# Kernel optimization log

Hardware: AMD Instinct MI355X
Metric: run time of the kernel (lower is better)

## Reference

```python
import jax, jax.numpy as jnp
import numpy as np

N, X_DIM, Y_DIM, HID = 1024, 128, 128, 256


def setup_inputs() -> dict:
    key = jax.random.key(0)
    ks = jax.random.split(key, 4)
    x = jax.random.normal(ks[0], (N, X_DIM), dtype=jnp.float32)
    y = jax.random.normal(ks[1], (N, Y_DIM), dtype=jnp.float32)
    # PyTorch Linear default init scale ~ 1/sqrt(fan_in)
    W1 = jax.random.normal(ks[2], (X_DIM + Y_DIM, HID), dtype=jnp.float32) / np.sqrt(X_DIM + Y_DIM)
    b1 = jnp.zeros((HID,), dtype=jnp.float32)
    W2 = jax.random.normal(ks[3], (HID, 1), dtype=jnp.float32) / np.sqrt(HID)
    b2 = jnp.zeros((1,), dtype=jnp.float32)
    return {"x_samples": x, "y_samples": y, "W1": W1, "b1": b1, "W2": W2, "b2": b2}


def reference(x_samples, y_samples, W1, b1, W2, b2):
    n = y_samples.shape[0]
    x_dim = x_samples.shape[-1]
    # F(concat(x, y)) on the diagonal pairs -> T0: [N, 1]
    xy = jnp.concatenate([x_samples, y_samples], axis=-1)
    T0 = jax.nn.relu(xy @ W1 + b1) @ W2 + b2
    # Pairwise term without materializing the [N, N, x+y] concat:
    # T1[i, j] = F(concat(x[j], y[i])) - 1. Split W1 into x- and y-blocks and
    # broadcast-sum the two small projections before the ReLU.
    Wx, Wy = W1[:x_dim], W1[x_dim:]
    xp = x_samples @ Wx  # [N, HID]
    yp = y_samples @ Wy  # [N, HID]
    h = jax.nn.relu(xp[None, :, :] + yp[:, None, :] + b1)  # [N, N, HID]
    T1 = h @ W2 + b2 - 1.0  # [N, N, 1]
    lse = jax.nn.logsumexp(T1, axis=1)  # [N, 1]
    lower_bound = T0.mean() - jnp.exp(lse - jnp.log(jnp.float32(n))).mean()
    return lower_bound
```

## Files before the change

### kernel.cpp

```cpp
#include <hip/hip_runtime.h>


#define N_S   1024
#define XD    128
#define HIDD  256
#define JBLK  16
#define IBLK  8
#define JTILE 256

__global__ __launch_bounds__(256) void proj_kernel(
    const float* __restrict__ x, const float* __restrict__ y,
    const float* __restrict__ W1, const float* __restrict__ b1,
    float* __restrict__ At, float* __restrict__ Yp) {
  const int k     = threadIdx.x;
  const int which = blockIdx.y;
  const int r0    = blockIdx.x * JBLK;

  __shared__ float s_in[JBLK][XD];
  const float* src = which ? y : x;
  for (int t = k; t < JBLK * XD; t += 256)
    s_in[t >> 7][t & 127] = src[r0 * XD + t];
  __syncthreads();

  const float* W = W1 + (which ? XD * HIDD : 0);
  float acc[JBLK];
  #pragma unroll
  for (int r = 0; r < JBLK; ++r) acc[r] = 0.f;

  #pragma unroll 4
  for (int d = 0; d < XD; ++d) {
    const float w = W[d * HIDD + k];
    #pragma unroll
    for (int r = 0; r < JBLK; ++r)
      acc[r] = fmaf(s_in[r][d], w, acc[r]);
  }

  if (which) {
    #pragma unroll
    for (int r = 0; r < JBLK; ++r) Yp[(r0 + r) * HIDD + k] = acc[r];
  } else {
    const float bk = b1[k];
    __shared__ float s_t[HIDD][JBLK + 1];
    #pragma unroll
    for (int r = 0; r < JBLK; ++r) s_t[k][r] = acc[r] + bk;
    __syncthreads();
    const int jj = k & (JBLK - 1);
    const int kk = k >> 4;
    #pragma unroll
    for (int m = 0; m < JBLK; ++m) {
      const int kr = m * 16 + kk;
      At[kr * N_S + r0 + jj] = s_t[kr][jj];
    }
  }
}

__global__ __launch_bounds__(256, 2) void pair_kernel(
    const float* __restrict__ At, const float* __restrict__ Yp,
    const float* __restrict__ W2, const float* __restrict__ b2,
    float2* __restrict__ partial) {
  const int tid = threadIdx.x;
  const int ib  = blockIdx.x >> 2;
  const int jt  = blockIdx.x & 3;
  const int i0  = ib * IBLK;
  const int j   = jt * JTILE + tid;

  __shared__ float s_row[HIDD][12];
  #pragma unroll
  for (int ii = 0; ii < IBLK; ++ii)
    s_row[tid][ii] = Yp[(i0 + ii) * HIDD + tid];
  s_row[tid][8] = W2[tid];
  __syncthreads();

  float acc[IBLK];
  #pragma unroll
  for (int ii = 0; ii < IBLK; ++ii) acc[ii] = 0.f;

  const float* ap = At + j;
  #pragma unroll 4
  for (int k = 0; k < HIDD; ++k) {
    const float  a  = ap[k * N_S];
    const float4 y0 = *(const float4*)&s_row[k][0];
    const float4 y1 = *(const float4*)&s_row[k][4];
    const float  w  = s_row[k][8];
    acc[0] = fmaf(fmaxf(a + y0.x, 0.f), w, acc[0]);
    acc[1] = fmaf(fmaxf(a + y0.y, 0.f), w, acc[1]);
    acc[2] = fmaf(fmaxf(a + y0.z, 0.f), w, acc[2]);
    acc[3] = fmaf(fmaxf(a + y0.w, 0.f), w, acc[3]);
    acc[4] = fmaf(fmaxf(a + y1.x, 0.f), w, acc[4]);
    acc[5] = fmaf(fmaxf(a + y1.y, 0.f), w, acc[5]);
    acc[6] = fmaf(fmaxf(a + y1.z, 0.f), w, acc[6]);
    acc[7] = fmaf(fmaxf(a + y1.w, 0.f), w, acc[7]);
  }

  const float bb = b2[0] - 1.0f;
  float esum = 0.f;
  #pragma unroll
  for (int ii = 0; ii < IBLK; ++ii) esum += __expf(acc[ii] + bb);

  float diag = 0.f;
  const int dd = j - i0;
  #pragma unroll
  for (int ii = 0; ii < IBLK; ++ii)
    if (dd == ii) diag = acc[ii];

  #pragma unroll
  for (int m = 32; m >= 1; m >>= 1) {
    esum += __shfl_xor(esum, m, 64);
    diag += __shfl_xor(diag, m, 64);
  }
  __shared__ float s_es[4], s_dg[4];
  const int wave = tid >> 6, lane = tid & 63;
  if (lane == 0) { s_es[wave] = esum; s_dg[wave] = diag; }
  __syncthreads();
  if (tid == 0)
    partial[blockIdx.x] = make_float2(s_es[0] + s_es[1] + s_es[2] + s_es[3],
                                      s_dg[0] + s_dg[1] + s_dg[2] + s_dg[3]);
}

__global__ __launch_bounds__(256) void finalize_kernel(
    const float2* __restrict__ partial, const float* __restrict__ b2,
    float* __restrict__ out) {
  const int tid = threadIdx.x;
  const float2 p0 = partial[tid];
  const float2 p1 = partial[tid + 256];
  double es = (double)p0.x + (double)p1.x;
  double dg = (double)p0.y + (double)p1.y;
  #pragma unroll
  for (int m = 32; m >= 1; m >>= 1) {
    es += __shfl_xor(es, m, 64);
    dg += __shfl_xor(dg, m, 64);
  }
  __shared__ double s_es[4], s_dg[4];
  const int wave = tid >> 6, lane = tid & 63;
  if (lane == 0) { s_es[wave] = es; s_dg[wave] = dg; }
  __syncthreads();
  if (tid == 0) {
    const double esT = s_es[0] + s_es[1] + s_es[2] + s_es[3];
    const double dgT = s_dg[0] + s_dg[1] + s_dg[2] + s_dg[3];
    const double n = (double)N_S;
    out[0] = (float)(dgT / n + (double)b2[0] - esT / (n * n));
  }
}

extern "C" void kernel_launch(void* const* d_in, const int* in_sizes, int n_in,
                              void* d_out, int out_size, void* d_ws, size_t ws_size,
                              hipStream_t stream) {
  const float* x  = (const float*)d_in[0];
  const float* y  = (const float*)d_in[1];
  const float* W1 = (const float*)d_in[2];
  const float* b1 = (const float*)d_in[3];
  const float* W2 = (const float*)d_in[4];
  const float* b2 = (const float*)d_in[5];

  float*  At      = (float*)d_ws;
  float*  Yp      = At + HIDD * N_S;
  float2* partial = (float2*)(Yp + N_S * HIDD);

  dim3 g1(N_S / JBLK, 2);
  proj_kernel<<<g1, 256, 0, stream>>>(x, y, W1, b1, At, Yp);
  pair_kernel<<<(N_S / IBLK) * (N_S / JTILE), 256, 0, stream>>>(At, Yp, W2, b2, partial);
  finalize_kernel<<<1, 256, 0, stream>>>(partial, b2, (float*)d_out);
}
```

Measured before the change: 107.3 us.

## Split ReLU into rank-one and abs terms, read Y projections via scalar loads

Uses relu(z) = 0.5*(z + |z|) so the linear part of the pairwise MLP becomes a rank-one term R[j] + C[i]. A new small kernel precomputes R and C as dot products with W2. The inner loop then does only an add plus an FMA with an abs operand modifier, instead of add, max and FMA. The y-projection is now stored transposed and read straight from global memory with block-uniform addresses, replacing the LDS staging; occupancy is raised to 4 blocks per SIMD. The cost is an extra kernel launch and a small extra pass over the projections.

```diff
diff --git a/kernel.cpp b/kernel.cpp
--- a/kernel.cpp
+++ b/kernel.cpp
@@ -1,17 +1,18 @@
 #include <hip/hip_runtime.h>
 
 
-#define N_S   1024
-#define XD    128
-#define HIDD  256
-#define JBLK  16
-#define IBLK  8
-#define JTILE 256
+#define N_S  1024
+#define XD   128
+#define HIDD 256
+#define JBLK 8
+#define IBLK 8
+#define JT   256
+#define JPT  1
 
 __global__ __launch_bounds__(256) void proj_kernel(
     const float* __restrict__ x, const float* __restrict__ y,
     const float* __restrict__ W1, const float* __restrict__ b1,
-    float* __restrict__ At, float* __restrict__ Yp) {
+    float* __restrict__ At, float* __restrict__ YpT) {
   const int k     = threadIdx.x;
   const int which = blockIdx.y;
   const int r0    = blockIdx.x * JBLK;
@@ -35,73 +36,77 @@
       acc[r] = fmaf(s_in[r][d], w, acc[r]);
   }
 
-  if (which) {
-    #pragma unroll
-    for (int r = 0; r < JBLK; ++r) Yp[(r0 + r) * HIDD + k] = acc[r];
-  } else {
-    const float bk = b1[k];
-    __shared__ float s_t[HIDD][JBLK + 1];
-    #pragma unroll
-    for (int r = 0; r < JBLK; ++r) s_t[k][r] = acc[r] + bk;
-    __syncthreads();
-    const int jj = k & (JBLK - 1);
-    const int kk = k >> 4;
-    #pragma unroll
-    for (int m = 0; m < JBLK; ++m) {
-      const int kr = m * 16 + kk;
-      At[kr * N_S + r0 + jj] = s_t[kr][jj];
-    }
+  const float bk = which ? 0.f : b1[k];
+  float* dst = which ? YpT : At;
+  __shared__ float s_t[HIDD][JBLK + 1];
+  #pragma unroll
+  for (int r = 0; r < JBLK; ++r) s_t[k][r] = acc[r] + bk;
+  __syncthreads();
+  const int jj = k & (JBLK - 1);
+  const int kk = k >> 3;
+  #pragma unroll
+  for (int m = 0; m < JBLK; ++m) {
+    const int kr = m * 32 + kk;
+    dst[kr * N_S + r0 + jj] = s_t[kr][jj];
   }
 }
 
-__global__ __launch_bounds__(256, 2) void pair_kernel(
-    const float* __restrict__ At, const float* __restrict__ Yp,
-    const float* __restrict__ W2, const float* __restrict__ b2,
+__global__ __launch_bounds__(256) void rank1_kernel(
+    const float* __restrict__ At, const float* __restrict__ YpT,
+    const float* __restrict__ W2, float* __restrict__ R, float* __restrict__ C) {
+  const int b = blockIdx.x;
+  const int j = (b & 3) * 256 + threadIdx.x;
+  const float* src = (b < 4) ? At : YpT;
+  float s0 = 0.f, s1 = 0.f, s2 = 0.f, s3 = 0.f;
+  #pragma unroll 4
+  for (int k = 0; k < HIDD; k += 4) {
+    s0 = fmaf(src[(k + 0) * N_S + j], W2[k + 0], s0);
+    s1 = fmaf(src[(k + 1) * N_S + j], W2[k + 1], s1);
+    s2 = fmaf(src[(k + 2) * N_S + j], W2[k + 2], s2);
+    s3 = fmaf(src[(k + 3) * N_S + j], W2[k + 3], s3);
+  }
+  ((b < 4) ? R : C)[j] = (s0 + s1) + (s2 + s3);
+}
+
+__global__ __launch_bounds__(256, 4) void pair2_kernel(
+    const float* __restrict__ At, const float* __restrict__ YpT,
+    const float* __restrict__ W2, const float* __restrict__ R,
+    const float* __restrict__ C, const float* __restrict__ b2,
     float2* __restrict__ partial) {
   const int tid = threadIdx.x;
   const int ib  = blockIdx.x >> 2;
   const int jt  = blockIdx.x & 3;
   const int i0  = ib * IBLK;
-  const int j   = jt * JTILE + tid;
-
-  __shared__ float s_row[HIDD][12];
-  #pragma unroll
-  for (int ii = 0; ii < IBLK; ++ii)
-    s_row[tid][ii] = Yp[(i0 + ii) * HIDD + tid];
-  s_row[tid][8] = W2[tid];
-  __syncthreads();
+  const int j   = jt * JT + tid;
 
   float acc[IBLK];
   #pragma unroll
   for (int ii = 0; ii < IBLK; ++ii) acc[ii] = 0.f;
 
   const float* ap = At + j;
-  #pragma unroll 4
+  #pragma unroll 8
   for (int k = 0; k < HIDD; ++k) {
-    const float  a  = ap[k * N_S];
-    const float4 y0 = *(const float4*)&s_row[k][0];
-    const float4 y1 = *(const float4*)&s_row[k][4];
-    const float  w  = s_row[k][8];
-    acc[0] = fmaf(fmaxf(a + y0.x, 0.f), w, acc[0]);
-    acc[1] = fmaf(fmaxf(a + y0.y, 0.f), w, acc[1]);
-    acc[2] = fmaf(fmaxf(a + y0.z, 0.f), w, acc[2]);
-    acc[3] = fmaf(fmaxf(a + y0.w, 0.f), w, acc[3]);
-    acc[4] = fmaf(fmaxf(a + y1.x, 0.f), w, acc[4]);
-    acc[5] = fmaf(fmaxf(a + y1.y, 0.f), w, acc[5]);
-    acc[6] = fmaf(fmaxf(a + y1.z, 0.f), w, acc[6]);
-    acc[7] = fmaf(fmaxf(a + y1.w, 0.f), w, acc[7]);
+    const float a = ap[k * N_S];
+    const float w = W2[k];
+    const float* cr = YpT + k * N_S + i0;
+    #pragma unroll
+    for (int ii = 0; ii < IBLK; ++ii) {
+      const float z = a + cr[ii];
+      acc[ii] = fmaf(fabsf(z), w, acc[ii]);
+    }
   }
 
   const float bb = b2[0] - 1.0f;
-  float esum = 0.f;
-  #pragma unroll
-  for (int ii = 0; ii < IBLK; ++ii) esum += __expf(acc[ii] + bb);
-
-  float diag = 0.f;
+  const float Rj = R[j];
+  float esum = 0.f, diag = 0.f;
   const int dd = j - i0;
   #pragma unroll
-  for (int ii = 0; ii < IBLK; ++ii)
-    if (dd == ii) diag = acc[ii];
+  for (int ii = 0; ii < IBLK; ++ii) {
+    const float Ci = C[i0 + ii];
+    const float t  = fmaf(0.5f, Rj + Ci + acc[ii], bb);
+    esum += __expf(t);
+    if (ii == dd) diag += t;
+  }
 
   #pragma unroll
   for (int m = 32; m >= 1; m >>= 1) {
@@ -118,13 +123,14 @@
 }
 
 __global__ __launch_bounds__(256) void finalize_kernel(
-    const float2* __restrict__ partial, const float* __restrict__ b2,
-    float* __restrict__ out) {
+    const float2* __restrict__ partial, float* __restrict__ out) {
   const int tid = threadIdx.x;
-  const float2 p0 = partial[tid];
-  const float2 p1 = partial[tid + 256];
-  double es = (double)p0.x + (double)p1.x;
-  double dg = (double)p0.y + (double)p1.y;
+  double es = 0.0, dg = 0.0;
+  #pragma unroll
+  for (int t = 0; t < 2; ++t) {
+    const float2 p = partial[tid + 256 * t];
+    es += (double)p.x; dg += (double)p.y;
+  }
   #pragma unroll
   for (int m = 32; m >= 1; m >>= 1) {
     es += __shfl_xor(es, m, 64);
@@ -138,7 +144,7 @@
     const double esT = s_es[0] + s_es[1] + s_es[2] + s_es[3];
     const double dgT = s_dg[0] + s_dg[1] + s_dg[2] + s_dg[3];
     const double n = (double)N_S;
-    out[0] = (float)(dgT / n + (double)b2[0] - esT / (n * n));
+    out[0] = (float)(dgT / n + 1.0 - esT / (n * n));
   }
 }
 
@@ -153,11 +159,14 @@
   const float* b2 = (const float*)d_in[5];
 
   float*  At      = (float*)d_ws;
-  float*  Yp      = At + HIDD * N_S;
-  float2* partial = (float2*)(Yp + N_S * HIDD);
+  float*  YpT     = At + HIDD * N_S;
+  float*  R       = YpT + HIDD * N_S;
+  float*  C       = R + N_S;
+  float2* partial = (float2*)(C + N_S);
 
   dim3 g1(N_S / JBLK, 2);
-  proj_kernel<<<g1, 256, 0, stream>>>(x, y, W1, b1, At, Yp);
-  pair_kernel<<<(N_S / IBLK) * (N_S / JTILE), 256, 0, stream>>>(At, Yp, W2, b2, partial);
-  finalize_kernel<<<1, 256, 0, stream>>>(partial, b2, (float*)d_out);
+  proj_kernel<<<g1, 256, 0, stream>>>(x, y, W1, b1, At, YpT);
+  rank1_kernel<<<8, 256, 0, stream>>>(At, YpT, W2, R, C);
+  pair2_kernel<<<(N_S / IBLK) * (N_S / JT), 256, 0, stream>>>(At, YpT, W2, R, C, b2, partial);
+  finalize_kernel<<<1, 256, 0, stream>>>(partial, (float*)d_out);
 }
```

New measurement: 156.9 us. 1.46x slower.
